# Performance work log

Hardware: AMD Instinct MI355X
Metric: run time of the kernel (lower is better)

## Reference

```python
import math
import jax, jax.numpy as jnp
import numpy as np

NUM_HEADS = 8
FACTOR = 5


def setup_inputs() -> dict:
    key = jax.random.key(0)
    ks = jax.random.split(key, 7)
    B, L, D = 4, 2048, 512
    sample_k = min(FACTOR * int(math.ceil(math.log(L))), L)  # 40
    return {
        "q": jax.random.normal(ks[0], (B, L, D), dtype=jnp.float32),
        "k": jax.random.normal(ks[1], (B, L, D), dtype=jnp.float32),
        "v": jax.random.normal(ks[2], (B, L, D), dtype=jnp.float32),
        "Wq": jax.random.normal(ks[3], (D, D), dtype=jnp.float32) * (1.0 / math.sqrt(D)),
        "Wk": jax.random.normal(ks[4], (D, D), dtype=jnp.float32) * (1.0 / math.sqrt(D)),
        "Wv": jax.random.normal(ks[5], (D, D), dtype=jnp.float32) * (1.0 / math.sqrt(D)),
        # replaces tf.random.uniform((S, sample_k), maxval=L) shared over (B, H)
        "k_sample_idx": jax.random.randint(ks[6], (L, sample_k), 0, L, dtype=jnp.int32),
    }


def reference(q, k, v, Wq, Wk, Wv, k_sample_idx):
    B, L, D = q.shape
    H = NUM_HEADS
    E = D // H

    # dense_q / dense_k / dense_v (no bias)
    qp = q @ Wq
    kp = k @ Wk
    vp = v @ Wv

    # NOTE: original code uses a raw reshape (B, H, L, E), not a transpose-based
    # head split; we reproduce that exactly.
    q_ = qp.reshape(B, H, L, E)
    k_ = kp.reshape(B, H, L, E)
    v_ = vp.reshape(B, H, L, E)

    u_q = min(FACTOR * int(math.ceil(math.log(L))), L)  # top_n selected queries
    # sample_k is k_sample_idx.shape[-1]

    # --- _prob_qk: sparse sampled QK scores ---
    # k_sample[b,h,l,s,e] = k_[b,h, k_sample_idx[l,s], e]   (B,H,L,sample_k,E)
    k_sample = k_[:, :, k_sample_idx]
    qk_sample = jnp.einsum("bhle,bhlse->bhls", q_, k_sample)  # (B,H,L,sample_k)

    # sparsity measure: max - mean (mean uses /L as in original)
    m = jnp.max(qk_sample, axis=-1) - jnp.sum(qk_sample, axis=-1) / L  # (B,H,L)
    _, m_top = jax.lax.top_k(m, u_q)  # (B,H,u_q) indices of active queries

    # q_reduce = q_[b,h,m_top]  -> full scores against all keys
    q_reduce = jnp.take_along_axis(q_, m_top[..., None], axis=2)  # (B,H,u_q,E)
    scores = jnp.einsum("bhue,bhle->bhul", q_reduce, k_)  # (B,H,u_q,L)
    scores = scores * (1.0 / math.sqrt(D // H))

    # --- initial context: masked (causal) => cumulative sum of v ---
    context = jnp.cumsum(v_, axis=2)  # (B,H,L,E)

    # --- update context at selected query positions ---
    # ProbMask: key position j is masked iff j > original query index
    mask = jnp.arange(L)[None, None, None, :] > m_top[..., None]  # (B,H,u_q,L)
    scores = jnp.where(mask, -jnp.inf, scores)
    attn = jax.nn.softmax(scores, axis=-1)
    ctx_upd = jnp.einsum("bhul,bhle->bhue", attn, v_)  # (B,H,u_q,E)

    bidx = jnp.arange(B)[:, None, None]
    hidx = jnp.arange(H)[None, :, None]
    context = context.at[bidx, hidx, m_top].set(ctx_upd)

    return context.reshape(B, L, D)
```

## Files before the change

kernel.cpp:

```cpp
#include <hip/hip_runtime.h>
#include <hip/hip_bf16.h>
#include <float.h>

constexpr int Bc = 4;
constexpr int Lc = 2048;
constexpr int Dc = 512;
constexpr int Hc = 8;
constexpr int Ec = 64;
constexpr int Sc = 40;
constexpr int Uc = 40;
constexpr int LEc = Lc * Ec;
constexpr int BHc = Bc * Hc;
constexpr int Mrows = Bc * Lc;

typedef __attribute__((ext_vector_type(8))) short s16x8;
typedef __attribute__((ext_vector_type(4))) float f32x4;
typedef unsigned int u32;

__device__ __forceinline__ short f2bf(float x) {
    unsigned u = __float_as_uint(x);
    unsigned r = (u + 0x7fffu + ((u >> 16) & 1u)) >> 16;
    return (short)r;
}
__device__ __forceinline__ float bf2f(short s) {
    return __uint_as_float(((unsigned)(unsigned short)s) << 16);
}
__device__ __forceinline__ uint4 pack8(const short* s) {
    uint4 r;
    r.x = (unsigned)(unsigned short)s[0] | ((unsigned)(unsigned short)s[1] << 16);
    r.y = (unsigned)(unsigned short)s[2] | ((unsigned)(unsigned short)s[3] << 16);
    r.z = (unsigned)(unsigned short)s[4] | ((unsigned)(unsigned short)s[5] << 16);
    r.w = (unsigned)(unsigned short)s[6] | ((unsigned)(unsigned short)s[7] << 16);
    return r;
}

__device__ __forceinline__ void gld_lds16(const short* g, short* l) {
    __builtin_amdgcn_global_load_lds(
        (const __attribute__((address_space(1))) u32*)g,
        (__attribute__((address_space(3))) u32*)l, 16, 0, 0);
}

__global__ __launch_bounds__(256) void split_inputs(
    const float* __restrict__ q, const float* __restrict__ k, const float* __restrict__ v,
    short* __restrict__ qhi, short* __restrict__ qlo,
    short* __restrict__ khi, short* __restrict__ klo, short* __restrict__ vhi)
{
    int tid = blockIdx.x * 256 + threadIdx.x;
    int z   = tid >> 19;
    int g8  = tid & ((1 << 19) - 1);
    int row = g8 >> 6;
    int gin = g8 & 63;
    int slot = (gin & ~7) | ((gin ^ row) & 7);
    const float* src = (z == 0) ? q : (z == 1) ? k : v;
    const float4* s4 = (const float4*)src + (size_t)g8 * 2;
    float4 d0 = s4[0], d1 = s4[1];
    float f[8] = {d0.x, d0.y, d0.z, d0.w, d1.x, d1.y, d1.z, d1.w};
    short hs[8], ls[8];
    #pragma unroll
    for (int i = 0; i < 8; ++i) {
        hs[i] = f2bf(f[i]);
        ls[i] = f2bf(f[i] - bf2f(hs[i]));
    }
    size_t off = (size_t)row * 512 + slot * 8;
    if (z == 2) { *(uint4*)(vhi + off) = pack8(hs); return; }
    if (z == 0) { *(uint4*)(qhi + off) = pack8(hs); *(uint4*)(qlo + off) = pack8(ls); }
    else        { *(uint4*)(khi + off) = pack8(hs); *(uint4*)(klo + off) = pack8(ls); }
}

__global__ __launch_bounds__(256) void wprep(
    const float* __restrict__ Wq, const float* __restrict__ Wk,
    const float* __restrict__ Wv,
    short* __restrict__ Bq, short* __restrict__ Bk, short* __restrict__ Bv)
{
    __shared__ float tile[64][65];
    int z = blockIdx.z;
    const float* W = (z == 0) ? Wq : (z == 1) ? Wk : Wv;
    int k0 = blockIdx.x * 64, n0 = blockIdx.y * 64;
    int t = threadIdx.x;
    #pragma unroll
    for (int i = 0; i < 4; ++i) {
        int c = i * 256 + t, row = c >> 4, qq = c & 15;
        float4 d = *(const float4*)(W + (size_t)(k0 + row) * Dc + n0 + qq * 4);
        tile[row][qq * 4 + 0] = d.x; tile[row][qq * 4 + 1] = d.y;
        tile[row][qq * 4 + 2] = d.z; tile[row][qq * 4 + 3] = d.w;
    }
    __syncthreads();
    int n = t >> 2, ks = (t & 3) * 16;
    int nglob = n0 + n;
    short hs[16], ls[16];
    #pragma unroll
    for (int j = 0; j < 16; ++j) {
        float x = tile[ks + j][n];
        short h = f2bf(x);
        hs[j] = h;
        ls[j] = f2bf(x - bf2f(h));
    }
    int G0 = (k0 + ks) >> 3;
    int s0 = (G0 & ~7) | ((G0 ^ nglob) & 7);
    int s1 = ((G0 + 1) & ~7) | (((G0 + 1) ^ nglob) & 7);
    if (z < 2) {
        short* Bx = (z == 0) ? Bq : Bk;
        size_t rb = (size_t)nglob * 1536;
        *(uint4*)(Bx + rb + s0 * 8)        = pack8(hs);
        *(uint4*)(Bx + rb + s1 * 8)        = pack8(hs + 8);
        *(uint4*)(Bx + rb + 512 + s0 * 8)  = pack8(ls);
        *(uint4*)(Bx + rb + 512 + s1 * 8)  = pack8(ls + 8);
        *(uint4*)(Bx + rb + 1024 + s0 * 8) = pack8(hs);
        *(uint4*)(Bx + rb + 1024 + s1 * 8) = pack8(hs + 8);
    } else {
        size_t rb = (size_t)nglob * 512;
        *(uint4*)(Bv + rb + s0 * 8) = pack8(hs);
        *(uint4*)(Bv + rb + s1 * 8) = pack8(hs + 8);
    }
}

__global__ __launch_bounds__(256) void gemm_mfma(
    const short* __restrict__ qhi, const short* __restrict__ qlo,
    const short* __restrict__ khi, const short* __restrict__ klo,
    const short* __restrict__ vhi,
    const short* __restrict__ Bq, const short* __restrict__ Bk,
    const short* __restrict__ Bv,
    float* __restrict__ qp, float* __restrict__ kp, float* __restrict__ vp)
{
    int z = blockIdx.z;
    const short* Ahi = (z == 0) ? qhi : (z == 1) ? khi : vhi;
    const short* Alo = (z == 0) ? qlo : (z == 1) ? klo : vhi;
    const short* Bx  = (z == 0) ? Bq  : (z == 1) ? Bk  : Bv;
    float* O = (z == 0) ? qp : (z == 1) ? kp : vp;
    const int Ktot = (z == 2) ? 512 : 1536;
    const int nseg = (z == 2) ? 1 : 3;

    __shared__ short As[128 * 64];
    __shared__ short Bs[128 * 64];

    const int t = threadIdx.x;
    const int lane = t & 63, w = t >> 6;
    const int wm = w >> 1, wn = w & 1;
    const int row0 = blockIdx.x * 128, col0 = blockIdx.y * 128;
    const int kg = lane >> 4, fr = lane & 15;
    const int sx = fr & 7;
    const int lrow = lane >> 3, lcol = (lane & 7) * 8;

    f32x4 acc[4][4];
    #pragma unroll
    for (int i = 0; i < 4; ++i)
        #pragma unroll
        for (int j = 0; j < 4; ++j)
            acc[i][j] = (f32x4){0.f, 0.f, 0.f, 0.f};

    for (int seg = 0; seg < nseg; ++seg) {
        const short* Asrc = ((seg == 2) ? Alo : Ahi)
                          + (size_t)(row0 + lrow) * 512 + lcol;
        const short* Bsrc = Bx + (size_t)(col0 + lrow) * Ktot + seg * 512 + lcol;
        for (int ks = 0; ks < 512; ks += 64) {
            __syncthreads();
            #pragma unroll
            for (int i = 0; i < 4; ++i) {
                int r = w * 32 + i * 8;
                gld_lds16(Asrc + (size_t)r * 512 + ks, &As[r * 64]);
            }
            #pragma unroll
            for (int i = 0; i < 4; ++i) {
                int r = w * 32 + i * 8;
                gld_lds16(Bsrc + (size_t)r * Ktot + ks, &Bs[r * 64]);
            }
            __syncthreads();

            #pragma unroll
            for (int kk = 0; kk < 2; ++kk) {
                const int slot = ((kk * 4 + kg) ^ sx) * 8;
                s16x8 a[4];
                #pragma unroll
                for (int mi = 0; mi < 4; ++mi)
                    a[mi] = *(const s16x8*)&As[(wm * 64 + mi * 16 + fr) * 64 + slot];
                #pragma unroll
                for (int ni = 0; ni < 4; ++ni) {
                    s16x8 b = *(const s16x8*)&Bs[(wn * 64 + ni * 16 + fr) * 64 + slot];
                    #pragma unroll
                    for (int mi = 0; mi < 4; ++mi)
                        acc[mi][ni] = __builtin_amdgcn_mfma_f32_16x16x32_bf16(a[mi], b, acc[mi][ni], 0, 0, 0);
                }
            }
        }
    }

    #pragma unroll
    for (int mi = 0; mi < 4; ++mi) {
        #pragma unroll
        for (int ni = 0; ni < 4; ++ni) {
            int row = row0 + wm * 64 + mi * 16 + (lane >> 4) * 4;
            int col = col0 + wn * 64 + ni * 16 + (lane & 15);
            #pragma unroll
            for (int r4 = 0; r4 < 4; ++r4)
                O[(size_t)(row + r4) * Dc + col] = acc[mi][ni][r4];
        }
    }
}

__global__ __launch_bounds__(256) void compute_m(
    const float* __restrict__ qp, const float* __restrict__ kp,
    const int* __restrict__ ksi, float* __restrict__ m_out)
{
    __shared__ float qsh[4][Ec];
    __shared__ int   jsh[4][Sc];
    int w    = threadIdx.x >> 6;
    int lane = threadIdx.x & 63;
    int xcd  = blockIdx.x & 7;
    int i    = blockIdx.x >> 3;
    int bh   = (xcd << 2) | (i >> 9);
    int l    = (i & 511) * 4 + w;
    const float* kbase = kp + (size_t)bh * LEc;

    qsh[w][lane] = qp[(size_t)bh * LEc + l * Ec + lane];
    if (lane < Sc) jsh[w][lane] = ksi[l * Sc + lane];
    __syncthreads();

    const int g = lane >> 2;
    const int c = lane & 3;

    float mx = -FLT_MAX, sm = 0.f;
    #pragma unroll
    for (int it = 0; it < 3; ++it) {
        int s = it * 16 + g;
        bool valid = (s < Sc);
        float partial = 0.f;
        if (valid) {
            int j = jsh[w][s];
            const float4* krow = (const float4*)(kbase + (size_t)j * Ec);
            #pragma unroll
            for (int ii = 0; ii < 4; ++ii) {
                float4 kv = krow[ii * 4 + c];
                float4 qv = *(const float4*)&qsh[w][ii * 16 + c * 4];
                partial += kv.x * qv.x + kv.y * qv.y + kv.z * qv.z + kv.w * qv.w;
            }
        }
        partial += __shfl_xor(partial, 1);
        partial += __shfl_xor(partial, 2);
        float vmax = valid ? partial : -FLT_MAX;
        float vsum = (valid && c == 0) ? partial : 0.f;
        #pragma unroll
        for (int o = 4; o < 64; o <<= 1) {
            vmax = fmaxf(vmax, __shfl_xor(vmax, o));
            vsum += __shfl_xor(vsum, o);
        }
        mx = fmaxf(mx, vmax);
        sm += vsum;
    }
    if (lane == 0) m_out[bh * Lc + l] = mx - sm * (1.0f / Lc);
}

__global__ __launch_bounds__(256) void topk40(
    const float* __restrict__ m_in, int* __restrict__ mtop)
{
    __shared__ float vals[Lc];
    __shared__ float wv[4];
    __shared__ int   wi[4];
    int bh = blockIdx.x, t = threadIdx.x;
    int lane = t & 63, w = t >> 6;
    for (int i = t; i < Lc; i += 256) vals[i] = m_in[bh * Lc + i];
    __syncthreads();
    for (int it = 0; it < Uc; ++it) {
        float lv = -FLT_MAX; int li = 0x7fffffff;
        #pragma unroll
        for (int rep = 0; rep < Lc / 256; ++rep) {
            int i = rep * 256 + t;
            float v = vals[i];
            if (v > lv) { lv = v; li = i; }
        }
        #pragma unroll
        for (int o = 1; o < 64; o <<= 1) {
            float ov = __shfl_xor(lv, o);
            int   oi = __shfl_xor(li, o);
            if (ov > lv || (ov == lv && oi < li)) { lv = ov; li = oi; }
        }
        if (lane == 0) { wv[w] = lv; wi[w] = li; }
        __syncthreads();
        if (t == 0) {
            float Bv = wv[0]; int Bi = wi[0];
            #pragma unroll
            for (int j = 1; j < 4; ++j) {
                if (wv[j] > Bv || (wv[j] == Bv && wi[j] < Bi)) { Bv = wv[j]; Bi = wi[j]; }
            }
            mtop[bh * Uc + it] = Bi;
            vals[Bi] = -FLT_MAX;
        }
        __syncthreads();
    }
}

constexpr int CH = 64;
constexpr int CR = 32;

__global__ __launch_bounds__(64) void cumsum_p1(
    const float* __restrict__ vp, float* __restrict__ psum)
{
    int bid = blockIdx.x;
    int e = threadIdx.x;
    int bh = bid >> 6, ch = bid & 63;
    const float* base = vp + (size_t)bh * LEc + (ch * CR) * Ec + e;
    float s = 0.f;
    #pragma unroll 8
    for (int r = 0; r < CR; ++r) s += base[r * Ec];
    psum[(size_t)bid * Ec + e] = s;
}

__global__ __launch_bounds__(64) void cumsum_p2(float* __restrict__ psum)
{
    int bh = blockIdx.x;
    int e = threadIdx.x;
    float off = 0.f;
    for (int c = 0; c < CH; ++c) {
        size_t idx = (size_t)(bh * CH + c) * Ec + e;
        float tv = psum[idx];
        psum[idx] = off;
        off += tv;
    }
}

__global__ __launch_bounds__(64) void cumsum_p3(
    const float* __restrict__ vp, const float* __restrict__ psum,
    float* __restrict__ out)
{
    int bid = blockIdx.x;
    int e = threadIdx.x;
    int bh = bid >> 6, ch = bid & 63;
    const float* base = vp  + (size_t)bh * LEc + (ch * CR) * Ec + e;
    float*       ob   = out + (size_t)bh * LEc + (ch * CR) * Ec + e;
    float run = psum[(size_t)bid * Ec + e];
    #pragma unroll 8
    for (int r = 0; r < CR; ++r) { run += base[r * Ec]; ob[r * Ec] = run; }
}

constexpr int ACH = 16;
constexpr int AROWS = 128;

__global__ __launch_bounds__(512) void attn_partial(
    const float* __restrict__ qp, const float* __restrict__ kp,
    const float* __restrict__ vp, const int* __restrict__ mtop,
    float* __restrict__ pl, float* __restrict__ pacc)
{
    __shared__ float Kt[64][68];
    __shared__ float Vt[64][68];
    __shared__ float qsh[40][64];
    __shared__ float p_lds[64][45];
    __shared__ int   lsel_sh[40];

    int half = blockIdx.x >> 8, sub = blockIdx.x & 255;
    int bh = sub & 31;
    int ch = half ? (15 - (sub >> 5)) : (sub >> 5);
    int t = threadIdx.x, w = t >> 6, lane = t & 63;
    const float* kb = kp + (size_t)bh * LEc;
    const float* vb = vp + (size_t)bh * LEc;

    if (t < Uc) lsel_sh[t] = mtop[bh * Uc + t];
    __syncthreads();
    for (int i = t; i < Uc * Ec; i += 512) {
        int u = i >> 6, e = i & 63;
        qsh[u][e] = qp[(size_t)bh * LEc + lsel_sh[u] * Ec + e];
    }

    const int u0 = w * 5;
    float acc[5]  = {0.f, 0.f, 0.f, 0.f, 0.f};
    float lreg[5] = {0.f, 0.f, 0.f, 0.f, 0.f};

    for (int tt = 0; tt < AROWS / 64; ++tt) {
        int l0 = ch * AROWS + tt * 64;
        __syncthreads();
        #pragma unroll
        for (int i = 0; i < 2; ++i) {
            int f = i * 512 + t, row = f >> 4, cg = f & 15;
            *(float4*)&Kt[row][cg * 4] = *(const float4*)(kb + (size_t)(l0 + row) * Ec + cg * 4);
            *(float4*)&Vt[row][cg * 4] = *(const float4*)(vb + (size_t)(l0 + row) * Ec + cg * 4);
        }
        __syncthreads();

        int gl = l0 + lane;
        float4 kr[16];
        #pragma unroll
        for (int i = 0; i < 16; ++i) kr[i] = *(const float4*)&Kt[lane][i * 4];

        bool act[5];
        #pragma unroll
        for (int j = 0; j < 5; ++j) {
            int u = u0 + j, ls = lsel_sh[u];
            act[j] = (l0 <= ls);
            if (!act[j]) continue;
            float p = 0.f;
            if (gl <= ls) {
                float dot = 0.f;
                #pragma unroll
                for (int i = 0; i < 16; ++i) {
                    float4 qv = *(const float4*)&qsh[u][i * 4];
                    dot += kr[i].x * qv.x + kr[i].y * qv.y + kr[i].z * qv.z + kr[i].w * qv.w;
                }
                p = __expf(dot * 0.125f);
            }
            p_lds[lane][u] = p;
            float ps = p;
            #pragma unroll
            for (int o = 1; o < 64; o <<= 1) ps += __shfl_xor(ps, o);
            lreg[j] += ps;
        }

        for (int row = 0; row < 64; ++row) {
            float vv = Vt[row][lane];
            #pragma unroll
            for (int j = 0; j < 5; ++j)
                if (act[j]) acc[j] = fmaf(p_lds[row][u0 + j], vv, acc[j]);
        }
    }

    #pragma unroll
    for (int j = 0; j < 5; ++j) {
        size_t idx = ((size_t)bh * ACH + ch) * Uc + u0 + j;
        if (lane == 0) pl[idx] = lreg[j];
        pacc[idx * Ec + lane] = acc[j];
    }
}

__global__ __launch_bounds__(256) void attn_combine(
    const float* __restrict__ pl, const float* __restrict__ pacc,
    const int* __restrict__ mtop, float* __restrict__ out)
{
    int wid = blockIdx.x * 4 + (threadIdx.x >> 6);
    int lane = threadIdx.x & 63;
    int bh = wid / Uc, u = wid % Uc;
    float l = 0.f, a = 0.f;
    for (int i = 0; i < ACH; ++i) {
        size_t idx = ((size_t)bh * ACH + i) * Uc + u;
        l += pl[idx];
        a += pacc[idx * Ec + lane];
    }
    int lsel = mtop[bh * Uc + u];
    out[(size_t)bh * LEc + lsel * Ec + lane] = a / l;
}

extern "C" void kernel_launch(void* const* d_in, const int* in_sizes, int n_in,
                              void* d_out, int out_size, void* d_ws, size_t ws_size,
                              hipStream_t stream)
{
    const float* q   = (const float*)d_in[0];
    const float* k   = (const float*)d_in[1];
    const float* v   = (const float*)d_in[2];
    const float* Wq  = (const float*)d_in[3];
    const float* Wk  = (const float*)d_in[4];
    const float* Wv  = (const float*)d_in[5];
    const int*   ksi = (const int*)d_in[6];
    float* out = (float*)d_out;

    float* wsf  = (float*)d_ws;
    float* qp   = wsf;
    float* kp   = qp + (size_t)Mrows * Dc;
    float* vp   = kp + (size_t)Mrows * Dc;
    float* psum = vp + (size_t)Mrows * Dc;
    float* m_ws = psum + (size_t)BHc * CH * Ec;
    int*   mtop = (int*)(m_ws + (size_t)BHc * Lc);
    short* qhi = (short*)(mtop + BHc * Uc);
    short* qlo = qhi + (size_t)Mrows * Dc;
    short* khi = qlo + (size_t)Mrows * Dc;
    short* klo = khi + (size_t)Mrows * Dc;
    short* vhi = klo + (size_t)Mrows * Dc;
    short* Bq  = vhi + (size_t)Mrows * Dc;
    short* Bk  = Bq + (size_t)Dc * 1536;
    short* Bv  = Bk + (size_t)Dc * 1536;
    float* pl  = (float*)(Bv + (size_t)Dc * 512);
    float* pacc = pl + (size_t)BHc * ACH * Uc;

    split_inputs<<<3 * (Mrows * Dc / 8) / 256, 256, 0, stream>>>(
        q, k, v, qhi, qlo, khi, klo, vhi);
    wprep<<<dim3(8, 8, 3), 256, 0, stream>>>(Wq, Wk, Wv, Bq, Bk, Bv);

    dim3 g1(Mrows / 128, Dc / 128, 3);
    gemm_mfma<<<g1, 256, 0, stream>>>(qhi, qlo, khi, klo, vhi, Bq, Bk, Bv,
                                      qp, kp, vp);

    compute_m<<<(BHc * Lc) / 4, 256, 0, stream>>>(qp, kp, ksi, m_ws);

    topk40<<<BHc, 256, 0, stream>>>(m_ws, mtop);

    attn_partial<<<BHc * ACH, 512, 0, stream>>>(qp, kp, vp, mtop, pl, pacc);

    cumsum_p1<<<BHc * CH, 64, 0, stream>>>(vp, psum);
    cumsum_p2<<<BHc, 64, 0, stream>>>(psum);
    cumsum_p3<<<BHc * CH, 64, 0, stream>>>(vp, psum, out);

    attn_combine<<<BHc * Uc / 4, 256, 0, stream>>>(pl, pacc, mtop, out);
}
```

Baseline: 179.2 us.

## Replace iterative argmax top-k with parallel rank counting and atomic scatter

The top-40 selection used 40 serial rounds of block-wide argmax, each with two barriers, on just 32 blocks. It now launches 8 blocks per (batch, head). Each thread computes its element's rank by comparing against all 2048 values in shared memory, and elements ranked below 40 are scattered through an atomic counter. This removes the serial barrier-bound loop but does O(L) compares per element, writes the indices in a nondeterministic order, and adds a memset plus an extra workspace counter.

Measured after the change: 198.0 us. 1.11x slower.

```diff
diff --git a/kernel.cpp b/kernel.cpp
--- a/kernel.cpp
+++ b/kernel.cpp
@@ -250,41 +250,24 @@
 }
 
 __global__ __launch_bounds__(256) void topk40(
-    const float* __restrict__ m_in, int* __restrict__ mtop)
+    const float* __restrict__ m_in, int* __restrict__ mtop, int* __restrict__ cnt)
 {
     __shared__ float vals[Lc];
-    __shared__ float wv[4];
-    __shared__ int   wi[4];
-    int bh = blockIdx.x, t = threadIdx.x;
-    int lane = t & 63, w = t >> 6;
+    int bh = blockIdx.x >> 3, seg = blockIdx.x & 7;
+    int t = threadIdx.x;
     for (int i = t; i < Lc; i += 256) vals[i] = m_in[bh * Lc + i];
     __syncthreads();
-    for (int it = 0; it < Uc; ++it) {
-        float lv = -FLT_MAX; int li = 0x7fffffff;
-        #pragma unroll
-        for (int rep = 0; rep < Lc / 256; ++rep) {
-            int i = rep * 256 + t;
-            float v = vals[i];
-            if (v > lv) { lv = v; li = i; }
-        }
-        #pragma unroll
-        for (int o = 1; o < 64; o <<= 1) {
-            float ov = __shfl_xor(lv, o);
-            int   oi = __shfl_xor(li, o);
-            if (ov > lv || (ov == lv && oi < li)) { lv = ov; li = oi; }
-        }
-        if (lane == 0) { wv[w] = lv; wi[w] = li; }
-        __syncthreads();
-        if (t == 0) {
-            float Bv = wv[0]; int Bi = wi[0];
-            #pragma unroll
-            for (int j = 1; j < 4; ++j) {
-                if (wv[j] > Bv || (wv[j] == Bv && wi[j] < Bi)) { Bv = wv[j]; Bi = wi[j]; }
-            }
-            mtop[bh * Uc + it] = Bi;
-            vals[Bi] = -FLT_MAX;
-        }
-        __syncthreads();
+    int myi = seg * 256 + t;
+    float vi = vals[myi];
+    int r = 0;
+    #pragma unroll 8
+    for (int j = 0; j < Lc; ++j) {
+        float vj = vals[j];
+        r += (vj > vi) || (vj == vi && j < myi);
+    }
+    if (r < Uc) {
+        int pos = atomicAdd(&cnt[bh], 1);
+        mtop[bh * Uc + pos] = myi;
     }
 }
 
@@ -465,6 +448,9 @@
     short* Bv  = Bk + (size_t)Dc * 1536;
     float* pl  = (float*)(Bv + (size_t)Dc * 512);
     float* pacc = pl + (size_t)BHc * ACH * Uc;
+    int*   cnt  = (int*)(pacc + (size_t)BHc * ACH * Uc * Ec);
+
+    hipMemsetAsync(cnt, 0, BHc * sizeof(int), stream);
 
     split_inputs<<<3 * (Mrows * Dc / 8) / 256, 256, 0, stream>>>(
         q, k, v, qhi, qlo, khi, klo, vhi);
@@ -476,7 +462,7 @@
 
     compute_m<<<(BHc * Lc) / 4, 256, 0, stream>>>(qp, kp, ksi, m_ws);
 
-    topk40<<<BHc, 256, 0, stream>>>(m_ws, mtop);
+    topk40<<<BHc * 8, 256, 0, stream>>>(m_ws, mtop, cnt);
 
     attn_partial<<<BHc * ACH, 512, 0, stream>>>(qp, kp, vp, mtop, pl, pacc);
 
```
